# Optimization experiments

Hardware: AMD Instinct MI355X
Metric: run time of the kernel (lower is better)

Reference implementation:

```python
import jax, jax.numpy as jnp
import numpy as np

N, M, D = 100000, 50000, 256
NE = N + M
B = 131072

def kl_normal_std(mu, scale):
    # KL( N(mu, scale) || N(0, 1) ) = -log(scale) + (scale^2 + mu^2)/2 - 1/2
    return 0.5 * (scale * scale + mu * mu - 1.0) - jnp.log(scale)

def setup_inputs() -> dict:
    key = jax.random.key(0)
    ks = jax.random.split(key, 8)
    users = jax.random.randint(ks[0], (B, 1), 0, N)
    items = jax.random.randint(ks[1], (B, 1), N, NE)
    x = jnp.concatenate([users, items], axis=1)                        # [B, 2]
    bias_table = jax.random.normal(ks[2], (NE, 2), dtype=jnp.float32)
    entity_table = jax.random.normal(ks[3], (NE, 2 * D), dtype=jnp.float32)
    global_bias_mean = jnp.zeros((1,), dtype=jnp.float32)
    global_bias_scale = jnp.ones((1,), dtype=jnp.float32)
    nb_occ = jax.random.randint(ks[4], (NE,), 1, 1001)                 # train occurrence counts >= 1
    eps_bias = jax.random.normal(ks[5], (NE,), dtype=jnp.float32)
    eps_entity = jax.random.normal(ks[6], (NE, D), dtype=jnp.float32)
    eps_global = jax.random.normal(ks[7], (1,), dtype=jnp.float32)
    return {"x": x, "bias_table": bias_table, "entity_table": entity_table,
            "global_bias_mean": global_bias_mean, "global_bias_scale": global_bias_scale,
            "nb_occ": nb_occ, "eps_bias": eps_bias, "eps_entity": eps_entity,
            "eps_global": eps_global}

def reference(x, bias_table, entity_table, global_bias_mean, global_bias_scale,
              nb_occ, eps_bias, eps_entity, eps_global):
    # --- reparameterized samples (one eps per table row == one eps per unique entity) ---
    gb_scale = jnp.abs(global_bias_scale)
    global_bias = global_bias_mean + gb_scale * eps_global             # [1]

    bias_mu = bias_table[:, 0]
    bias_sc = jnp.abs(bias_table[:, 1])
    biases_all = bias_mu + bias_sc * eps_bias                          # [NE]

    ent_mu = entity_table[:, :D]
    ent_sc = jnp.abs(entity_table[:, D:])
    entities_all = ent_mu + ent_sc * eps_entity                        # [NE, D]

    # --- FM forward: bias sum + product-sum interaction ---
    pair_bias = biases_all[x].sum(axis=1)                              # [B]
    pair_emb = (entities_all[x[:, 0]] * entities_all[x[:, 1]]).sum(axis=1)  # [B]
    logits = global_bias + pair_bias + pair_emb                        # [B] (Bernoulli logits)

    # --- closed-form KL vs N(0,1), rescaled by batch/train occupancy ---
    kl_bias = kl_normal_std(bias_mu, bias_sc)                          # [NE]
    kl_entity = kl_normal_std(ent_mu, ent_sc).sum(axis=1)              # [NE]

    nb_occ_f = nb_occ.astype(jnp.float32)
    cnt = jnp.bincount(x.reshape(-1), length=NE).astype(jnp.float32)   # nb_occ_in_batch
    cnt_u = jnp.bincount(x[:, 0], length=NE).astype(jnp.float32)
    cnt_i = jnp.bincount(x[:, 1], length=NE).astype(jnp.float32)
    user_norm = (cnt_u / nb_occ_f).sum()
    item_norm = (cnt_i / nb_occ_f).sum()

    ids = jnp.arange(NE)
    scale_term = (jnp.where(ids <= N, float(N), 0.0) / user_norm
                  + jnp.where(ids > N, float(M), 0.0) / item_norm)
    kl_rescaled = ((kl_bias + kl_entity) * (cnt / nb_occ_f) * scale_term).sum()

    kl_global = kl_normal_std(global_bias_mean, gb_scale).sum()
    return logits, kl_global + kl_rescaled
```

## Files before the change

kernel.cpp:

```cpp
#include <hip/hip_runtime.h>
#include <math.h>

#define NU   100000
#define MI   50000
#define NEn  150000
#define Bp   131072

typedef float f4v __attribute__((ext_vector_type(4)));

__device__ __forceinline__ float wred(float v) {
#pragma unroll
    for (int m = 32; m > 0; m >>= 1) v += __shfl_xor(v, m, 64);
    return v;
}

__global__ __launch_bounds__(256) void k_count(const int* __restrict__ x,
                                               int* __restrict__ cnt,
                                               const float* __restrict__ gbm,
                                               const float* __restrict__ gbs,
                                               float* __restrict__ outkl) {
    int t = blockIdx.x * 256 + threadIdx.x;
    if (t < 2 * Bp) atomicAdd(cnt + x[t], 1);
    if (t == 0) {
        float gm = gbm[0];
        float gs = fabsf(gbs[0]);
        outkl[0] = 0.5f * (gs * gs + gm * gm - 1.0f) - __logf(gs);
    }
}

__global__ __launch_bounds__(256) void k_entity(
    const f4v* __restrict__ et,
    const f4v* __restrict__ epse,
    const float* __restrict__ bt,
    const float* __restrict__ epsb,
    const int*   __restrict__ cnt,
    f4v*   __restrict__ ent,
    float* __restrict__ biases,
    float* __restrict__ klpe)
{
    int lane = threadIdx.x & 63;
    int e    = blockIdx.x * 4 + (threadIdx.x >> 6);
    if (cnt[e] == 0) return;

    const f4v* row = et + (size_t)e * 128;
    f4v mu = __builtin_nontemporal_load(row + lane);
    f4v s4 = __builtin_nontemporal_load(row + 64 + lane);
    f4v ep = __builtin_nontemporal_load(epse + (size_t)e * 64 + lane);
    float scx = fabsf(s4.x), scy = fabsf(s4.y), scz = fabsf(s4.z), scw = fabsf(s4.w);

    if (ent) {
        f4v o;
        o.x = fmaf(scx, ep.x, mu.x);
        o.y = fmaf(scy, ep.y, mu.y);
        o.z = fmaf(scz, ep.z, mu.z);
        o.w = fmaf(scw, ep.w, mu.w);
        ent[(size_t)e * 64 + lane] = o;
    }

    float kl = 0.5f * (scx * scx + mu.x * mu.x - 1.0f) - __logf(scx)
             + 0.5f * (scy * scy + mu.y * mu.y - 1.0f) - __logf(scy)
             + 0.5f * (scz * scz + mu.z * mu.z - 1.0f) - __logf(scz)
             + 0.5f * (scw * scw + mu.w * mu.w - 1.0f) - __logf(scw);
    kl = wred(kl);

    if (lane == 0) {
        float bmu = bt[2 * e];
        float bsc = fabsf(bt[2 * e + 1]);
        biases[e] = fmaf(bsc, epsb[e], bmu);
        klpe[e]   = kl + 0.5f * (bsc * bsc + bmu * bmu - 1.0f) - __logf(bsc);
    }
}

__global__ __launch_bounds__(256) void k_norms(
    const int* __restrict__ cnt, const int* __restrict__ nb,
    float* __restrict__ hdr)
{
    int e = blockIdx.x * 256 + threadIdx.x;
    float uv = 0.f, iv = 0.f;
    if (e < NEn) {
        float v = (float)cnt[e] / (float)nb[e];
        if (e < NU) uv = v; else iv = v;
    }
    uv = wred(uv);
    iv = wred(iv);
    if ((threadIdx.x & 63) == 0) {
        if (uv != 0.f) atomicAdd(hdr + 0, uv);
        if (iv != 0.f) atomicAdd(hdr + 1, iv);
    }
}

__global__ __launch_bounds__(256) void k_logits(
    const int* __restrict__ x, const float4* __restrict__ ent,
    const float* __restrict__ biases,
    const float* __restrict__ gbm, const float* __restrict__ gbs,
    const float* __restrict__ epsg, float* __restrict__ out)
{
    int lane = threadIdx.x & 63;
    int p    = blockIdx.x * 4 + (threadIdx.x >> 6);
    int u = x[2 * p], v = x[2 * p + 1];
    float4 a = ent[(size_t)u * 64 + lane];
    float4 b = ent[(size_t)v * 64 + lane];
    float d = a.x * b.x + a.y * b.y + a.z * b.z + a.w * b.w;
    d = wred(d);
    if (lane == 0) {
        float gb = fmaf(fabsf(gbs[0]), epsg[0], gbm[0]);
        out[p] = gb + biases[u] + biases[v] + d;
    }
}

__global__ __launch_bounds__(256) void k_logits_rc(
    const int* __restrict__ x, const float4* __restrict__ et,
    const float4* __restrict__ epse, const float* __restrict__ biases,
    const float* __restrict__ gbm, const float* __restrict__ gbs,
    const float* __restrict__ epsg, float* __restrict__ out)
{
    int lane = threadIdx.x & 63;
    int p    = blockIdx.x * 4 + (threadIdx.x >> 6);
    int u = x[2 * p], v = x[2 * p + 1];
    const float4* ru = et + (size_t)u * 128;
    const float4* rv = et + (size_t)v * 128;
    float4 mu_u = ru[lane], s_u = ru[64 + lane], e_u = epse[(size_t)u * 64 + lane];
    float4 mu_v = rv[lane], s_v = rv[64 + lane], e_v = epse[(size_t)v * 64 + lane];
    float ax = fmaf(fabsf(s_u.x), e_u.x, mu_u.x), bx = fmaf(fabsf(s_v.x), e_v.x, mu_v.x);
    float ay = fmaf(fabsf(s_u.y), e_u.y, mu_u.y), by = fmaf(fabsf(s_v.y), e_v.y, mu_v.y);
    float az = fmaf(fabsf(s_u.z), e_u.z, mu_u.z), bz = fmaf(fabsf(s_v.z), e_v.z, mu_v.z);
    float aw = fmaf(fabsf(s_u.w), e_u.w, mu_u.w), bw = fmaf(fabsf(s_v.w), e_v.w, mu_v.w);
    float d = ax * bx + ay * by + az * bz + aw * bw;
    d = wred(d);
    if (lane == 0) {
        float gb = fmaf(fabsf(gbs[0]), epsg[0], gbm[0]);
        out[p] = gb + biases[u] + biases[v] + d;
    }
}

__global__ __launch_bounds__(256) void k_klred(
    const float* __restrict__ klpe, const int* __restrict__ cnt,
    const int* __restrict__ nb, const float* __restrict__ hdr,
    float* __restrict__ outkl)
{
    int e = blockIdx.x * 256 + threadIdx.x;
    float t = 0.f;
    if (e < NEn) {
        int c = cnt[e];
        if (c != 0) {
            float sc = (e <= NU) ? ((float)NU / hdr[0]) : ((float)MI / hdr[1]);
            t = klpe[e] * ((float)c / (float)nb[e]) * sc;
        }
    }
    t = wred(t);
    if ((threadIdx.x & 63) == 0 && t != 0.f) atomicAdd(outkl, t);
}

extern "C" void kernel_launch(void* const* d_in, const int* in_sizes, int n_in,
                              void* d_out, int out_size, void* d_ws, size_t ws_size,
                              hipStream_t stream)
{
    const int*   x    = (const int*)d_in[0];
    const float* bt   = (const float*)d_in[1];
    const float* et   = (const float*)d_in[2];
    const float* gbm  = (const float*)d_in[3];
    const float* gbs  = (const float*)d_in[4];
    const int*   nb   = (const int*)d_in[5];
    const float* epsb = (const float*)d_in[6];
    const float* epse = (const float*)d_in[7];
    const float* epsg = (const float*)d_in[8];
    float* out = (float*)d_out;

    char*  ws   = (char*)d_ws;
    float* hdr  = (float*)ws;
    int*   cnt  = (int*)  (ws + 64);
    float* klpe = (float*)(ws + 64 + (size_t)NEn * 4);
    float* bia  = (float*)(ws + 64 + (size_t)NEn * 8);
    size_t entoff = 64 + (size_t)NEn * 12;
    float4* ent = nullptr;
    if (ws_size >= entoff + (size_t)NEn * 256 * 4)
        ent = (float4*)(ws + entoff);

    (void)hipMemsetAsync(ws, 0, 64 + (size_t)NEn * 4, stream);

    k_count <<<(2 * Bp + 255) / 256, 256, 0, stream>>>(x, cnt, gbm, gbs, out + Bp);
    k_entity<<<NEn / 4,              256, 0, stream>>>((const f4v*)et,
                                                       (const f4v*)epse,
                                                       bt, epsb, cnt, (f4v*)ent, bia, klpe);
    k_norms <<<(NEn + 255) / 256,    256, 0, stream>>>(cnt, nb, hdr);
    if (ent)
        k_logits   <<<Bp / 4, 256, 0, stream>>>(x, ent, bia, gbm, gbs, epsg, out);
    else
        k_logits_rc<<<Bp / 4, 256, 0, stream>>>(x, (const float4*)et,
                                                (const float4*)epse, bia,
                                                gbm, gbs, epsg, out);
    k_klred <<<(NEn + 255) / 256,    256, 0, stream>>>(klpe, cnt, nb, hdr, out + Bp);
}
```

Before: 603.2 us.

## Fuse all stages into one persistent cooperative kernel with grid syncs

Replaces the memset plus five separate launches (count, entity sampling/KL, norms, logits, KL reduction) with a single cooperative kernel. It uses grid-stride loops and grid.sync barriers between phases, and folds the norm accumulation into the entity pass. It also moves the KL reduction ahead of the logits phase, so the logits phase starts without an extra barrier. The aim is to cut launch overhead and the tail bubbles between kernels. The trade-offs are the cost of grid-wide barriers and persistent-grid scheduling, which may use memory bandwidth less efficiently than the one-wave-per-row launches. The original multi-kernel path remains as a fallback.

```diff
diff --git a/kernel.cpp b/kernel.cpp
--- a/kernel.cpp
+++ b/kernel.cpp
@@ -1,5 +1,8 @@
 #include <hip/hip_runtime.h>
+#include <hip/hip_cooperative_groups.h>
 #include <math.h>
+
+namespace cg = cooperative_groups;
 
 #define NU   100000
 #define MI   50000
@@ -7,11 +10,147 @@
 #define Bp   131072
 
 typedef float f4v __attribute__((ext_vector_type(4)));
+typedef int   i2v __attribute__((ext_vector_type(2)));
 
 __device__ __forceinline__ float wred(float v) {
 #pragma unroll
     for (int m = 32; m > 0; m >>= 1) v += __shfl_xor(v, m, 64);
     return v;
+}
+
+struct MegaArgs {
+    const int*   x;
+    const float* bt;
+    const f4v*   et;
+    const float* gbm;
+    const float* gbs;
+    const int*   nb;
+    const float* epsb;
+    const f4v*   epse;
+    const float* epsg;
+    int*   cnt;
+    float* hdr;
+    float* klpe;
+    float* bia;
+    f4v*   ent;
+    float* out;
+};
+
+__global__ __launch_bounds__(256, 8) void mega(MegaArgs a) {
+    cg::grid_group grid = cg::this_grid();
+    const int tid  = threadIdx.x;
+    const int lane = tid & 63;
+    const int wib  = tid >> 6;
+    const int nthr = (int)gridDim.x * 256;
+    const int gtid = (int)blockIdx.x * 256 + tid;
+    const int nwav = nthr >> 6;
+    const int gwav = (int)blockIdx.x * 4 + wib;
+
+    __shared__ float su[4], si[4], sk[4];
+
+    for (int i = gtid; i < NEn; i += nthr) a.cnt[i] = 0;
+    if (gtid < 2) a.hdr[gtid] = 0.f;
+    grid.sync();
+
+    for (int t = gtid; t < 2 * Bp; t += nthr) atomicAdd(a.cnt + a.x[t], 1);
+    if (gtid == 0) {
+        float gm = a.gbm[0], gs = fabsf(a.gbs[0]);
+        a.out[Bp] = 0.5f * (gs * gs + gm * gm - 1.0f) - __logf(gs);
+    }
+    grid.sync();
+
+    float uacc = 0.f, iacc = 0.f;
+    for (int e = gwav; e < NEn; e += nwav) {
+        int c = a.cnt[e];
+        if (lane == 0) {
+            float v = (float)c / (float)a.nb[e];
+            if (e < NU) uacc += v; else iacc += v;
+        }
+        if (c == 0) continue;
+
+        const f4v* row = a.et + (size_t)e * 128;
+        f4v mu = __builtin_nontemporal_load(row + lane);
+        f4v s4 = __builtin_nontemporal_load(row + 64 + lane);
+        f4v ep = __builtin_nontemporal_load(a.epse + (size_t)e * 64 + lane);
+        float scx = fabsf(s4.x), scy = fabsf(s4.y), scz = fabsf(s4.z), scw = fabsf(s4.w);
+
+        if (a.ent) {
+            f4v o;
+            o.x = fmaf(scx, ep.x, mu.x);
+            o.y = fmaf(scy, ep.y, mu.y);
+            o.z = fmaf(scz, ep.z, mu.z);
+            o.w = fmaf(scw, ep.w, mu.w);
+            a.ent[(size_t)e * 64 + lane] = o;
+        }
+
+        float kl = 0.5f * (scx * scx + mu.x * mu.x - 1.0f) - __logf(scx)
+                 + 0.5f * (scy * scy + mu.y * mu.y - 1.0f) - __logf(scy)
+                 + 0.5f * (scz * scz + mu.z * mu.z - 1.0f) - __logf(scz)
+                 + 0.5f * (scw * scw + mu.w * mu.w - 1.0f) - __logf(scw);
+        kl = wred(kl);
+
+        if (lane == 0) {
+            float bmu = a.bt[2 * e];
+            float bsc = fabsf(a.bt[2 * e + 1]);
+            a.bia[e]  = fmaf(bsc, a.epsb[e], bmu);
+            a.klpe[e] = kl + 0.5f * (bsc * bsc + bmu * bmu - 1.0f) - __logf(bsc);
+        }
+    }
+    if (lane == 0) { su[wib] = uacc; si[wib] = iacc; }
+    __syncthreads();
+    if (tid == 0) {
+        float u = su[0] + su[1] + su[2] + su[3];
+        float i = si[0] + si[1] + si[2] + si[3];
+        if (u != 0.f) atomicAdd(a.hdr + 0, u);
+        if (i != 0.f) atomicAdd(a.hdr + 1, i);
+    }
+    grid.sync();
+
+    const float un  = a.hdr[0];
+    const float itn = a.hdr[1];
+    float kt = 0.f;
+    for (int e = gtid; e < NEn; e += nthr) {
+        int c = a.cnt[e];
+        if (c != 0) {
+            float sc = (e <= NU) ? ((float)NU / un) : ((float)MI / itn);
+            kt += a.klpe[e] * ((float)c / (float)a.nb[e]) * sc;
+        }
+    }
+    kt = wred(kt);
+    if (lane == 0) sk[wib] = kt;
+    __syncthreads();
+    if (tid == 0) {
+        float s = sk[0] + sk[1] + sk[2] + sk[3];
+        if (s != 0.f) atomicAdd(a.out + Bp, s);
+    }
+
+    const float gb = fmaf(fabsf(a.gbs[0]), a.epsg[0], a.gbm[0]);
+    const bool use_ent = (a.ent != nullptr);
+    for (int p = gwav; p < Bp; p += nwav) {
+        i2v pr = __builtin_nontemporal_load((const i2v*)a.x + p);
+        int u = pr.x, v = pr.y;
+        float d;
+        if (use_ent) {
+            f4v ea = a.ent[(size_t)u * 64 + lane];
+            f4v eb = a.ent[(size_t)v * 64 + lane];
+            d = ea.x * eb.x + ea.y * eb.y + ea.z * eb.z + ea.w * eb.w;
+        } else {
+            const f4v* ru = a.et + (size_t)u * 128;
+            const f4v* rv = a.et + (size_t)v * 128;
+            f4v mu_u = ru[lane], s_u = ru[64 + lane], e_u = a.epse[(size_t)u * 64 + lane];
+            f4v mu_v = rv[lane], s_v = rv[64 + lane], e_v = a.epse[(size_t)v * 64 + lane];
+            float ax = fmaf(fabsf(s_u.x), e_u.x, mu_u.x), bx = fmaf(fabsf(s_v.x), e_v.x, mu_v.x);
+            float ay = fmaf(fabsf(s_u.y), e_u.y, mu_u.y), by = fmaf(fabsf(s_v.y), e_v.y, mu_v.y);
+            float az = fmaf(fabsf(s_u.z), e_u.z, mu_u.z), bz = fmaf(fabsf(s_v.z), e_v.z, mu_v.z);
+            float aw = fmaf(fabsf(s_u.w), e_u.w, mu_u.w), bw = fmaf(fabsf(s_v.w), e_v.w, mu_v.w);
+            d = ax * bx + ay * by + az * bz + aw * bw;
+        }
+        d = wred(d);
+        if (lane == 0) {
+            float r = gb + a.bia[u] + a.bia[v] + d;
+            __builtin_nontemporal_store(r, a.out + p);
+        }
+    }
 }
 
 __global__ __launch_bounds__(256) void k_count(const int* __restrict__ x,
@@ -29,14 +168,10 @@
 }
 
 __global__ __launch_bounds__(256) void k_entity(
-    const f4v* __restrict__ et,
-    const f4v* __restrict__ epse,
-    const float* __restrict__ bt,
-    const float* __restrict__ epsb,
-    const int*   __restrict__ cnt,
-    f4v*   __restrict__ ent,
-    float* __restrict__ biases,
-    float* __restrict__ klpe)
+    const f4v* __restrict__ et, const f4v* __restrict__ epse,
+    const float* __restrict__ bt, const float* __restrict__ epsb,
+    const int* __restrict__ cnt, f4v* __restrict__ ent,
+    float* __restrict__ biases, float* __restrict__ klpe)
 {
     int lane = threadIdx.x & 63;
     int e    = blockIdx.x * 4 + (threadIdx.x >> 6);
@@ -172,19 +307,35 @@
     float* klpe = (float*)(ws + 64 + (size_t)NEn * 4);
     float* bia  = (float*)(ws + 64 + (size_t)NEn * 8);
     size_t entoff = 64 + (size_t)NEn * 12;
-    float4* ent = nullptr;
-    if (ws_size >= entoff + (size_t)NEn * 256 * 4)
-        ent = (float4*)(ws + entoff);
+    f4v* ent = nullptr;
+    if (ws_size >= entoff + (size_t)NEn * 1024)
+        ent = (f4v*)(ws + entoff);
+
+    MegaArgs a;
+    a.x = x; a.bt = bt; a.et = (const f4v*)et; a.gbm = gbm; a.gbs = gbs;
+    a.nb = nb; a.epsb = epsb; a.epse = (const f4v*)epse; a.epsg = epsg;
+    a.cnt = cnt; a.hdr = hdr; a.klpe = klpe; a.bia = bia; a.ent = ent; a.out = out;
+
+    int bpc = 0;
+    if (hipOccupancyMaxActiveBlocksPerMultiprocessor(&bpc, mega, 256, 0) != hipSuccess)
+        bpc = 0;
+    if (bpc > 8) bpc = 8;
+
+    if (bpc > 0) {
+        int grid = bpc * 256;
+        void* params[] = { (void*)&a };
+        if (hipLaunchCooperativeKernel(mega, dim3(grid), dim3(256),
+                                       params, 0u, stream) == hipSuccess)
+            return;
+    }
 
     (void)hipMemsetAsync(ws, 0, 64 + (size_t)NEn * 4, stream);
-
     k_count <<<(2 * Bp + 255) / 256, 256, 0, stream>>>(x, cnt, gbm, gbs, out + Bp);
-    k_entity<<<NEn / 4,              256, 0, stream>>>((const f4v*)et,
-                                                       (const f4v*)epse,
-                                                       bt, epsb, cnt, (f4v*)ent, bia, klpe);
+    k_entity<<<NEn / 4,              256, 0, stream>>>((const f4v*)et, (const f4v*)epse,
+                                                       bt, epsb, cnt, ent, bia, klpe);
     k_norms <<<(NEn + 255) / 256,    256, 0, stream>>>(cnt, nb, hdr);
     if (ent)
-        k_logits   <<<Bp / 4, 256, 0, stream>>>(x, ent, bia, gbm, gbs, epsg, out);
+        k_logits   <<<Bp / 4, 256, 0, stream>>>(x, (const float4*)ent, bia, gbm, gbs, epsg, out);
     else
         k_logits_rc<<<Bp / 4, 256, 0, stream>>>(x, (const float4*)et,
                                                 (const float4*)epse, bia,
```

Result: slower. 934.1 us (+54.8%).

## Store sampled embeddings in fp16 and fuse norm/KL-reduce kernels into neighbors

Applied to the files above, without the earlier changes.

The sampled entity embeddings are now written to the workspace as fp16 instead of fp32, which halves the intermediate write and the gather traffic in the logits kernel. Each wavefront now handles two pairs using 16-byte fp16 loads. The norms kernel is merged into the entity kernel and the KL reduction into the logits kernel as extra blocks, which removes two launches. The cost is fp16 rounding in the dot products, which may exceed tolerance.

```diff
diff --git a/kernel.cpp b/kernel.cpp
--- a/kernel.cpp
+++ b/kernel.cpp
@@ -6,11 +6,18 @@
 #define NEn  150000
 #define Bp   131072
 
-typedef float f4v __attribute__((ext_vector_type(4)));
+typedef float    f4v __attribute__((ext_vector_type(4)));
+typedef _Float16 h8v __attribute__((ext_vector_type(8)));
+typedef _Float16 h4v __attribute__((ext_vector_type(4)));
 
 __device__ __forceinline__ float wred(float v) {
 #pragma unroll
     for (int m = 32; m > 0; m >>= 1) v += __shfl_xor(v, m, 64);
+    return v;
+}
+__device__ __forceinline__ float hred(float v) {
+#pragma unroll
+    for (int m = 16; m > 0; m >>= 1) v += __shfl_xor(v, m, 64);
     return v;
 }
 
@@ -28,16 +35,34 @@
     }
 }
 
-__global__ __launch_bounds__(256) void k_entity(
+__global__ __launch_bounds__(256) void k_entnorm(
     const f4v* __restrict__ et,
     const f4v* __restrict__ epse,
     const float* __restrict__ bt,
     const float* __restrict__ epsb,
     const int*   __restrict__ cnt,
-    f4v*   __restrict__ ent,
+    const int*   __restrict__ nb,
+    h4v*   __restrict__ enth,
     float* __restrict__ biases,
-    float* __restrict__ klpe)
-{
+    float* __restrict__ klpe,
+    float* __restrict__ hdr)
+{
+    if (blockIdx.x >= NEn / 4) {
+        int e = (blockIdx.x - NEn / 4) * 256 + threadIdx.x;
+        float uv = 0.f, iv = 0.f;
+        if (e < NEn) {
+            float v = (float)cnt[e] / (float)nb[e];
+            if (e < NU) uv = v; else iv = v;
+        }
+        uv = wred(uv);
+        iv = wred(iv);
+        if ((threadIdx.x & 63) == 0) {
+            if (uv != 0.f) atomicAdd(hdr + 0, uv);
+            if (iv != 0.f) atomicAdd(hdr + 1, iv);
+        }
+        return;
+    }
+
     int lane = threadIdx.x & 63;
     int e    = blockIdx.x * 4 + (threadIdx.x >> 6);
     if (cnt[e] == 0) return;
@@ -48,13 +73,15 @@
     f4v ep = __builtin_nontemporal_load(epse + (size_t)e * 64 + lane);
     float scx = fabsf(s4.x), scy = fabsf(s4.y), scz = fabsf(s4.z), scw = fabsf(s4.w);
 
-    if (ent) {
-        f4v o;
-        o.x = fmaf(scx, ep.x, mu.x);
-        o.y = fmaf(scy, ep.y, mu.y);
-        o.z = fmaf(scz, ep.z, mu.z);
-        o.w = fmaf(scw, ep.w, mu.w);
-        ent[(size_t)e * 64 + lane] = o;
+    if (enth) {
+        float ox = fmaf(scx, ep.x, mu.x);
+        float oy = fmaf(scy, ep.y, mu.y);
+        float oz = fmaf(scz, ep.z, mu.z);
+        float ow = fmaf(scw, ep.w, mu.w);
+        h4v oh;
+        oh.x = (_Float16)ox; oh.y = (_Float16)oy;
+        oh.z = (_Float16)oz; oh.w = (_Float16)ow;
+        enth[(size_t)e * 64 + lane] = oh;
     }
 
     float kl = 0.5f * (scx * scx + mu.x * mu.x - 1.0f) - __logf(scx)
@@ -71,40 +98,46 @@
     }
 }
 
-__global__ __launch_bounds__(256) void k_norms(
-    const int* __restrict__ cnt, const int* __restrict__ nb,
-    float* __restrict__ hdr)
-{
-    int e = blockIdx.x * 256 + threadIdx.x;
-    float uv = 0.f, iv = 0.f;
-    if (e < NEn) {
-        float v = (float)cnt[e] / (float)nb[e];
-        if (e < NU) uv = v; else iv = v;
-    }
-    uv = wred(uv);
-    iv = wred(iv);
-    if ((threadIdx.x & 63) == 0) {
-        if (uv != 0.f) atomicAdd(hdr + 0, uv);
-        if (iv != 0.f) atomicAdd(hdr + 1, iv);
-    }
-}
-
-__global__ __launch_bounds__(256) void k_logits(
-    const int* __restrict__ x, const float4* __restrict__ ent,
+__global__ __launch_bounds__(256) void k_logred(
+    const int* __restrict__ x,
+    const h8v* __restrict__ enth,
     const float* __restrict__ biases,
     const float* __restrict__ gbm, const float* __restrict__ gbs,
-    const float* __restrict__ epsg, float* __restrict__ out)
-{
+    const float* __restrict__ epsg,
+    const float* __restrict__ klpe, const int* __restrict__ cnt,
+    const int* __restrict__ nb, const float* __restrict__ hdr,
+    float* __restrict__ out)
+{
+    if (blockIdx.x >= Bp / 8) {
+        int e = (blockIdx.x - Bp / 8) * 256 + threadIdx.x;
+        float t = 0.f;
+        if (e < NEn) {
+            int c = cnt[e];
+            if (c != 0) {
+                float sc = (e <= NU) ? ((float)NU / hdr[0]) : ((float)MI / hdr[1]);
+                t = klpe[e] * ((float)c / (float)nb[e]) * sc;
+            }
+        }
+        t = wred(t);
+        if ((threadIdx.x & 63) == 0 && t != 0.f) atomicAdd(out + Bp, t);
+        return;
+    }
+
     int lane = threadIdx.x & 63;
-    int p    = blockIdx.x * 4 + (threadIdx.x >> 6);
+    int sub  = lane & 31;
+    int p    = blockIdx.x * 8 + ((threadIdx.x >> 6) << 1) + (lane >> 5);
     int u = x[2 * p], v = x[2 * p + 1];
-    float4 a = ent[(size_t)u * 64 + lane];
-    float4 b = ent[(size_t)v * 64 + lane];
-    float d = a.x * b.x + a.y * b.y + a.z * b.z + a.w * b.w;
-    d = wred(d);
-    if (lane == 0) {
+    float bu = biases[u];
+    float bv = biases[v];
+    h8v a = enth[(size_t)u * 32 + sub];
+    h8v b = enth[(size_t)v * 32 + sub];
+    float d = 0.f;
+#pragma unroll
+    for (int i = 0; i < 8; ++i) d = fmaf((float)a[i], (float)b[i], d);
+    d = hred(d);
+    if (sub == 0) {
         float gb = fmaf(fabsf(gbs[0]), epsg[0], gbm[0]);
-        out[p] = gb + biases[u] + biases[v] + d;
+        out[p] = gb + bu + bv + d;
     }
 }
 
@@ -172,22 +205,28 @@
     float* klpe = (float*)(ws + 64 + (size_t)NEn * 4);
     float* bia  = (float*)(ws + 64 + (size_t)NEn * 8);
     size_t entoff = 64 + (size_t)NEn * 12;
-    float4* ent = nullptr;
-    if (ws_size >= entoff + (size_t)NEn * 256 * 4)
-        ent = (float4*)(ws + entoff);
+    h4v* enth = nullptr;
+    if (ws_size >= entoff + (size_t)NEn * 512)
+        enth = (h4v*)(ws + entoff);
+
+    const int NORMB = (NEn + 255) / 256;
 
     (void)hipMemsetAsync(ws, 0, 64 + (size_t)NEn * 4, stream);
 
-    k_count <<<(2 * Bp + 255) / 256, 256, 0, stream>>>(x, cnt, gbm, gbs, out + Bp);
-    k_entity<<<NEn / 4,              256, 0, stream>>>((const f4v*)et,
-                                                       (const f4v*)epse,
-                                                       bt, epsb, cnt, (f4v*)ent, bia, klpe);
-    k_norms <<<(NEn + 255) / 256,    256, 0, stream>>>(cnt, nb, hdr);
-    if (ent)
-        k_logits   <<<Bp / 4, 256, 0, stream>>>(x, ent, bia, gbm, gbs, epsg, out);
-    else
+    k_count<<<(2 * Bp + 255) / 256, 256, 0, stream>>>(x, cnt, gbm, gbs, out + Bp);
+
+    k_entnorm<<<NEn / 4 + NORMB, 256, 0, stream>>>(
+        (const f4v*)et, (const f4v*)epse, bt, epsb, cnt, nb,
+        enth, bia, klpe, hdr);
+
+    if (enth) {
+        k_logred<<<Bp / 8 + NORMB, 256, 0, stream>>>(
+            x, (const h8v*)enth, bia, gbm, gbs, epsg,
+            klpe, cnt, nb, hdr, out);
+    } else {
         k_logits_rc<<<Bp / 4, 256, 0, stream>>>(x, (const float4*)et,
                                                 (const float4*)epse, bia,
                                                 gbm, gbs, epsg, out);
-    k_klred <<<(NEn + 255) / 256,    256, 0, stream>>>(klpe, cnt, nb, hdr, out + Bp);
-}
+        k_klred<<<NORMB, 256, 0, stream>>>(klpe, cnt, nb, hdr, out + Bp);
+    }
+}
```

After: 572.7 us. -5.1%, faster.
